# Kernel tuning notes

Measured on AMD Instinct MI355X. Metric: run time of the kernel, lower is better.

Reference implementation:

```python
import jax, jax.numpy as jnp
import numpy as np

FEATURES = 1024
NUM_HEADS = 16
HEAD_DIM = FEATURES // NUM_HEADS


def _cinit(key, shape):
    # complex_xavier_init from the source: std = sqrt(1/(fan_in + fan_out))
    fan_in = int(np.prod(shape[:-1]))
    fan_out = shape[-1]
    std = np.sqrt(1.0 / (fan_in + fan_out)).astype(np.float32)
    return jax.random.normal(key, shape, dtype=jnp.float32) * std


def setup_inputs() -> dict:
    key = jax.random.key(0)
    ks = jax.random.split(key, 12)
    B, S, F = 2, 2048, FEATURES
    inp = {
        'x_r': jax.random.normal(ks[0], (B, S, F), dtype=jnp.float32),
        'x_i': jax.random.normal(ks[1], (B, S, F), dtype=jnp.float32),
        'mask': jnp.ones((B, S), dtype=jnp.float32),
    }
    names = ['q', 'k', 'v', 'o']
    for idx, n in enumerate(names):
        inp[f'W{n}_r'] = _cinit(ks[2 + 2 * idx], (F, F))
        inp[f'W{n}_i'] = _cinit(ks[3 + 2 * idx], (F, F))
        inp[f'b{n}_r'] = jnp.zeros((F,), dtype=jnp.float32)
        inp[f'b{n}_i'] = jnp.zeros((F,), dtype=jnp.float32)
    return inp


def _complex_linear(xr, xi, Wr, Wi, br, bi):
    # (xr + i xi) @ (Wr + i Wi) + (br + i bi)
    yr = xr @ Wr - xi @ Wi + br
    yi = xr @ Wi + xi @ Wr + bi
    return yr, yi


def reference(x_r, x_i, mask,
              Wq_r, Wq_i, bq_r, bq_i,
              Wk_r, Wk_i, bk_r, bk_i,
              Wv_r, Wv_i, bv_r, bv_i,
              Wo_r, Wo_i, bo_r, bo_i):
    B, S, F = x_r.shape
    H, D = NUM_HEADS, HEAD_DIM

    Qr, Qi = _complex_linear(x_r, x_i, Wq_r, Wq_i, bq_r, bq_i)
    Kr, Ki = _complex_linear(x_r, x_i, Wk_r, Wk_i, bk_r, bk_i)
    Vr, Vi = _complex_linear(x_r, x_i, Wv_r, Wv_i, bv_r, bv_i)

    def split_heads(t):  # [B,S,F] -> [B,H,S,D]
        return t.reshape(B, S, H, D).transpose(0, 2, 1, 3)

    Qr, Qi, Kr, Ki, Vr, Vi = map(split_heads, (Qr, Qi, Kr, Ki, Vr, Vi))

    scale = 1.0 / jnp.sqrt(jnp.float32(D))
    # Re(Q K^H) = Qr.Kr + Qi.Ki
    scores = (jnp.einsum('bhqd,bhkd->bhqk', Qr, Kr)
              + jnp.einsum('bhqd,bhkd->bhqk', Qi, Ki)) * scale
    scores = scores + (1.0 - mask[:, None, None, :]) * -1e9
    attn = jax.nn.softmax(scores, axis=-1)  # real-valued weights

    out_r = jnp.einsum('bhqk,bhkd->bhqd', attn, Vr)
    out_i = jnp.einsum('bhqk,bhkd->bhqd', attn, Vi)

    def merge_heads(t):  # [B,H,S,D] -> [B,S,F]
        return t.transpose(0, 2, 1, 3).reshape(B, S, F)

    out_r, out_i = merge_heads(out_r), merge_heads(out_i)
    out_r, out_i = _complex_linear(out_r, out_i, Wo_r, Wo_i, bo_r, bo_i)
    # stack real/imag parts: [2, B, S, F]
    return jnp.stack([out_r, out_i], axis=0)
```

## Files before the change

### kernel.cpp

```cpp
#include <hip/hip_runtime.h>
#include <hip/hip_bf16.h>

typedef unsigned short u16;
typedef unsigned int   u32;
typedef __attribute__((ext_vector_type(8))) short bf16x8;
typedef __attribute__((ext_vector_type(4))) float f32x4;

#define FDIM 1024
#define NH   16
#define HD   64
#define SEQ  2048

#define MFMA16 __builtin_amdgcn_mfma_f32_16x16x32_bf16

__device__ __forceinline__ u16 f2bf(float f) {
    __hip_bfloat16 h = __float2bfloat16(f);
    return *reinterpret_cast<u16*>(&h);
}

__device__ __forceinline__ void g2l16(const u16* g, u16* l) {
    __builtin_amdgcn_global_load_lds(
        (const __attribute__((address_space(1))) unsigned int*)g,
        (__attribute__((address_space(3))) unsigned int*)l,
        16, 0, 0);
}

__global__ __launch_bounds__(256)
void convert_x(const float* __restrict__ xr, const float* __restrict__ xi,
               u16* __restrict__ dr, u16* __restrict__ di)
{
    const long n4 = (long)2 * SEQ * FDIM / 4;
    for (long i = (long)blockIdx.x * blockDim.x + threadIdx.x; i < n4;
         i += (long)gridDim.x * blockDim.x) {
        float4 v = ((const float4*)xr)[i];
        ushort4 o;
        o.x = f2bf(v.x); o.y = f2bf(v.y); o.z = f2bf(v.z); o.w = f2bf(v.w);
        ((ushort4*)dr)[i] = o;
        v = ((const float4*)xi)[i];
        o.x = f2bf(v.x); o.y = f2bf(v.y); o.z = f2bf(v.z); o.w = f2bf(v.w);
        ((ushort4*)di)[i] = o;
    }
}

__global__ __launch_bounds__(256)
void convert_w(const float* __restrict__ W0, const float* __restrict__ W1,
               const float* __restrict__ W2, const float* __restrict__ W3,
               const float* __restrict__ W4, const float* __restrict__ W5,
               const float* __restrict__ W6, const float* __restrict__ W7,
               u16* __restrict__ wt_base)
{
    __shared__ u16 T[64][68];
    const int z = blockIdx.z;
    const float* W = (z == 0) ? W0 : (z == 1) ? W1 : (z == 2) ? W2 : (z == 3) ? W3
                   : (z == 4) ? W4 : (z == 5) ? W5 : (z == 6) ? W6 : W7;
    u16* Wt = wt_base + (long)z * FDIM * FDIM;
    const int n0 = blockIdx.x * 64, k0 = blockIdx.y * 64;
    const int tid = threadIdx.x;
    const int cr = tid & 15, rr = tid >> 4;
    #pragma unroll
    for (int p = 0; p < 4; p++) {
        const int k = p * 16 + rr;
        float4 v = *(const float4*)&W[(long)(k0 + k) * FDIM + n0 + cr * 4];
        T[k][cr*4 + 0] = f2bf(v.x); T[k][cr*4 + 1] = f2bf(v.y);
        T[k][cr*4 + 2] = f2bf(v.z); T[k][cr*4 + 3] = f2bf(v.w);
    }
    __syncthreads();
    #pragma unroll
    for (int p = 0; p < 4; p++) {
        const int n = p * 16 + rr;
        ushort4 o;
        o.x = T[cr*4 + 0][n]; o.y = T[cr*4 + 1][n];
        o.z = T[cr*4 + 2][n]; o.w = T[cr*4 + 3][n];
        *(ushort4*)&Wt[(long)(n0 + n) * FDIM + k0 + cr*4] = o;
    }
}

__global__ __launch_bounds__(256)
void proj_bf16(const u16* __restrict__ Xr_g, const u16* __restrict__ Xi_g,
               const u16* __restrict__ Wt_base,
               const float* __restrict__ bqr, const float* __restrict__ bqi,
               const float* __restrict__ bkr, const float* __restrict__ bki,
               const float* __restrict__ bvr, const float* __restrict__ bvi,
               u16* __restrict__ ws)
{
    __shared__ u16 XsR[2][128 * 32], XsI[2][128 * 32];
    __shared__ u16 WsR[2][128 * 32], WsI[2][128 * 32];

    const int z = blockIdx.z, t = z % 3, b = z / 3;
    const u16* xr = Xr_g + (long)b * SEQ * FDIM;
    const u16* xi = Xi_g + (long)b * SEQ * FDIM;
    const long WT = (long)FDIM * FDIM;
    const u16* wr = Wt_base + (long)(2 * t) * WT;
    const u16* wi = wr + WT;
    const float* br = (t == 0) ? bqr : (t == 1) ? bkr : bvr;
    const float* bi = (t == 0) ? bqi : (t == 1) ? bki : bvi;
    const long TS = (long)2 * SEQ * FDIM;
    u16* outR = ws + (long)(t * 2) * TS + (long)b * SEQ * FDIM;
    u16* outI = outR + TS;

    const int tid = threadIdx.x;
    const int n0  = blockIdx.x * 128;
    const int m0  = blockIdx.y * 128;

    const int lane = tid & 63;
    const int wv   = tid >> 6;
    const int mwo  = (wv >> 1) * 64;
    const int nwo  = (wv & 1) * 64;
    const int ml   = lane & 15;
    const int kg   = lane >> 4;

    const int lr = lane >> 2;
    const int xc = (((lane & 3) ^ (lr & 3)) * 8);
    const int rc = ((kg ^ (ml & 3)) * 8);

    f32x4 accr[4][4], acci[4][4];
    #pragma unroll
    for (int i = 0; i < 4; i++)
        #pragma unroll
        for (int j = 0; j < 4; j++) { accr[i][j] = (f32x4)(0.0f); acci[i][j] = (f32x4)(0.0f); }

    #define PSTAGE(bufi, kk)                                                     \
        do {                                                                     \
            _Pragma("unroll")                                                    \
            for (int sub = 0; sub < 2; sub++) {                                  \
                const int rs  = wv * 32 + sub * 16;                              \
                const int row = rs + lr;                                         \
                g2l16(xr + (long)(m0 + row) * FDIM + (kk) + xc, &XsR[bufi][rs * 32]); \
                g2l16(xi + (long)(m0 + row) * FDIM + (kk) + xc, &XsI[bufi][rs * 32]); \
                g2l16(wr + (long)(n0 + row) * FDIM + (kk) + xc, &WsR[bufi][rs * 32]); \
                g2l16(wi + (long)(n0 + row) * FDIM + (kk) + xc, &WsI[bufi][rs * 32]); \
            }                                                                    \
        } while (0)

    int buf = 0;
    PSTAGE(0, 0);
    __syncthreads();

    for (int k0 = 0; k0 < FDIM; k0 += 32) {
        if (k0 + 32 < FDIM) PSTAGE(buf ^ 1, k0 + 32);

        bf16x8 ar[4], ai[4], nai[4], brf[4], bif[4];
        #pragma unroll
        for (int i = 0; i < 4; i++) {
            ar[i] = *(const bf16x8*)&XsR[buf][(mwo + 16*i + ml) * 32 + rc];
            union { bf16x8 v; u32 w[4]; } u;
            u.v = *(const bf16x8*)&XsI[buf][(mwo + 16*i + ml) * 32 + rc];
            ai[i] = u.v;
            u.w[0] ^= 0x80008000u; u.w[1] ^= 0x80008000u;
            u.w[2] ^= 0x80008000u; u.w[3] ^= 0x80008000u;
            nai[i] = u.v;
        }
        #pragma unroll
        for (int j = 0; j < 4; j++) {
            brf[j] = *(const bf16x8*)&WsR[buf][(nwo + 16*j + ml) * 32 + rc];
            bif[j] = *(const bf16x8*)&WsI[buf][(nwo + 16*j + ml) * 32 + rc];
        }
        #pragma unroll
        for (int i = 0; i < 4; i++)
            #pragma unroll
            for (int j = 0; j < 4; j++) {
                accr[i][j] = MFMA16(ar[i],  brf[j], accr[i][j], 0, 0, 0);
                accr[i][j] = MFMA16(nai[i], bif[j], accr[i][j], 0, 0, 0);
                acci[i][j] = MFMA16(ar[i],  bif[j], acci[i][j], 0, 0, 0);
                acci[i][j] = MFMA16(ai[i],  brf[j], acci[i][j], 0, 0, 0);
            }

        __syncthreads();
        buf ^= 1;
    }
    #undef PSTAGE

    #pragma unroll
    for (int j = 0; j < 4; j++) {
        const int n = n0 + nwo + 16*j + ml;
        const int hh = n >> 6, d = n & 63;
        const float bre = br[n];
        const float bim = bi[n];
        #pragma unroll
        for (int i = 0; i < 4; i++) {
            const int mb = m0 + mwo + 16*i + kg*4;
            if (t < 2) {
                #pragma unroll
                for (int r = 0; r < 4; r++) {
                    const long addr = ((long)hh * SEQ + (mb + r)) * HD + d;
                    outR[addr] = f2bf(accr[i][j][r] + bre);
                    outI[addr] = f2bf(acci[i][j][r] + bim);
                }
            } else {
                const long addr = ((long)hh * HD + d) * SEQ + mb;
                ushort4 vr, vi;
                vr.x = f2bf(accr[i][j][0] + bre); vr.y = f2bf(accr[i][j][1] + bre);
                vr.z = f2bf(accr[i][j][2] + bre); vr.w = f2bf(accr[i][j][3] + bre);
                vi.x = f2bf(acci[i][j][0] + bim); vi.y = f2bf(acci[i][j][1] + bim);
                vi.z = f2bf(acci[i][j][2] + bim); vi.w = f2bf(acci[i][j][3] + bim);
                *(ushort4*)&outR[addr] = vr;
                *(ushort4*)&outI[addr] = vi;
            }
        }
    }
}

__global__ __launch_bounds__(256)
void attn_mfma(const u16* __restrict__ Qr_g, const u16* __restrict__ Qi_g,
               const u16* __restrict__ Kr_g, const u16* __restrict__ Ki_g,
               const u16* __restrict__ Vtr_g, const u16* __restrict__ Vti_g,
               const float* __restrict__ mask_g,
               u16* __restrict__ Ar_g, u16* __restrict__ Ai_g)
{
    __shared__ u16 KT[2][64 * 128];
    __shared__ u16 VT[2][128 * 64];

    const int tid  = threadIdx.x;
    const int lane = tid & 63;
    const int wv   = tid >> 6;
    const int ml   = lane & 15;
    const int quad = lane >> 4;

    const int L   = blockIdx.x + (blockIdx.y << 4) + (blockIdx.z << 8);
    const int xcd = L & 7, qq = L >> 3;
    const int q0  = (qq & 15) * 128;
    const int g   = ((qq >> 4) << 3) | xcd;
    const int h   = g & 15;
    const int b   = g >> 4;
    const long hb  = ((long)b * NH + h) * SEQ * HD;
    const float* mask = mask_g + (long)b * SEQ;

    bf16x8 qf[2][4];
    #pragma unroll
    for (int nt = 0; nt < 2; nt++) {
        const long row = hb + (long)(q0 + wv*32 + nt*16 + ml) * HD;
        qf[nt][0] = *(const bf16x8*)(Qr_g + row + quad*8);
        qf[nt][1] = *(const bf16x8*)(Qr_g + row + 32 + quad*8);
        qf[nt][2] = *(const bf16x8*)(Qi_g + row + quad*8);
        qf[nt][3] = *(const bf16x8*)(Qi_g + row + 32 + quad*8);
    }

    const u16* srcK[4];
    #pragma unroll
    for (int ii = 0; ii < 4; ii++) {
        const int rk = wv*16 + ii*4 + (lane >> 4);
        const int c  = (lane & 15) ^ (rk & 7);
        srcK[ii] = ((c < 8) ? Kr_g : Ki_g) + hb + (long)rk * HD + (c & 7) * 8;
    }
    const u16* srcV[4];
    #pragma unroll
    for (int jj = 0; jj < 4; jj++) {
        const int dv = wv*32 + jj*8 + (lane >> 3);
        const int c  = (lane & 7) ^ (dv & 7);
        srcV[jj] = ((dv < 64) ? Vtr_g : Vti_g) + hb + (long)(dv & 63) * SEQ + c * 8;
    }

    #define STAGE(bufi)                                                         \
        do {                                                                    \
            _Pragma("unroll")                                                   \
            for (int ii = 0; ii < 4; ii++)                                      \
                g2l16(srcK[ii], &KT[bufi][(wv*16 + ii*4) * 128]);               \
            _Pragma("unroll")                                                   \
            for (int jj = 0; jj < 4; jj++)                                      \
                g2l16(srcV[jj], &VT[bufi][(wv*32 + jj*8) * 64]);                \
            _Pragma("unroll")                                                   \
            for (int ii = 0; ii < 4; ii++) srcK[ii] += 64 * HD;                 \
            _Pragma("unroll")                                                   \
            for (int jj = 0; jj < 4; jj++) srcV[jj] += 64;                      \
        } while (0)

    f32x4 oacc[2][8];
    #pragma unroll
    for (int mt = 0; mt < 2; mt++)
        #pragma unroll
        for (int nt = 0; nt < 8; nt++) oacc[mt][nt] = (f32x4)(0.0f);
    float m_run[2] = {-3.0e38f, -3.0e38f};
    float l_run[2] = {0.0f, 0.0f};
    const float scale = 0.125f;

    STAGE(0);
    __syncthreads();

    const int NT = SEQ / 64;
    for (int t = 0; t < NT; ++t) {
        const int cur = t & 1;
        if (t + 1 < NT) STAGE(cur ^ 1);

        f32x4 mrow[4];
        #pragma unroll
        for (int mt = 0; mt < 4; mt++)
            mrow[mt] = *(const f32x4*)(mask + t*64 + mt*16 + quad*4);

        f32x4 sacc[4][2];
        #pragma unroll
        for (int mt = 0; mt < 4; mt++) { sacc[mt][0] = (f32x4)(0.0f); sacc[mt][1] = (f32x4)(0.0f); }
        const u16* Kc = &KT[cur][0];
        __builtin_amdgcn_s_setprio(1);
        #pragma unroll
        for (int mt = 0; mt < 4; mt++)
            #pragma unroll
            for (int kc = 0; kc < 4; kc++) {
                const bf16x8 kf = *(const bf16x8*)
                    &Kc[(mt*16 + ml) * 128 + (((kc*4 + quad) ^ (ml & 7)) * 8)];
                sacc[mt][0] = MFMA16(kf, qf[0][kc], sacc[mt][0], 0, 0, 0);
                sacc[mt][1] = MFMA16(kf, qf[1][kc], sacc[mt][1], 0, 0, 0);
            }
        __builtin_amdgcn_s_setprio(0);

        asm volatile("s_barrier" ::: "memory");

        float md[4][4];
        #pragma unroll
        for (int mt = 0; mt < 4; mt++)
            #pragma unroll
            for (int r = 0; r < 4; r++)
                md[mt][r] = (1.0f - mrow[mt][r]) * -1.0e9f;

        u16* Pb = (u16*)&KT[cur][0];
        float alSave[2];
        #pragma unroll
        for (int nt = 0; nt < 2; nt++) {
            float sv[4][4];
            #pragma unroll
            for (int mt = 0; mt < 4; mt++)
                #pragma unroll
                for (int r = 0; r < 4; r++)
                    sv[mt][r] = sacc[mt][nt][r] * scale + md[mt][r];

            float mA = fmaxf(fmaxf(sv[0][0], sv[0][1]), fmaxf(sv[0][2], sv[0][3]));
            float mB = fmaxf(fmaxf(sv[1][0], sv[1][1]), fmaxf(sv[1][2], sv[1][3]));
            float mC = fmaxf(fmaxf(sv[2][0], sv[2][1]), fmaxf(sv[2][2], sv[2][3]));
            float mD = fmaxf(fmaxf(sv[3][0], sv[3][1]), fmaxf(sv[3][2], sv[3][3]));
            float mx = fmaxf(fmaxf(mA, mB), fmaxf(mC, mD));
            mx = fmaxf(mx, __shfl_xor(mx, 16));
            mx = fmaxf(mx, __shfl_xor(mx, 32));
            const float mn = fmaxf(m_run[nt], mx);
            const float al = __expf(m_run[nt] - mn);

            float p[4][4];
            #pragma unroll
            for (int mt = 0; mt < 4; mt++) {
                p[mt][0] = __expf(sv[mt][0] - mn);
                p[mt][1] = __expf(sv[mt][1] - mn);
                p[mt][2] = __expf(sv[mt][2] - mn);
                p[mt][3] = __expf(sv[mt][3] - mn);
            }
            const int qrow = wv*32 + nt*16 + ml;
            #pragma unroll
            for (int mt = 0; mt < 4; mt++) {
                ushort4 pb;
                pb.x = f2bf(p[mt][0]); pb.y = f2bf(p[mt][1]);
                pb.z = f2bf(p[mt][2]); pb.w = f2bf(p[mt][3]);
                *(ushort4*)&Pb[(long)qrow * 64
                               + (((mt*2 + (quad >> 1)) ^ (ml & 7)) * 8)
                               + (quad & 1) * 4] = pb;
            }
            float s0 = (p[0][0] + p[0][1]) + (p[0][2] + p[0][3]);
            float s1 = (p[1][0] + p[1][1]) + (p[1][2] + p[1][3]);
            float s2 = (p[2][0] + p[2][1]) + (p[2][2] + p[2][3]);
            float s3 = (p[3][0] + p[3][1]) + (p[3][2] + p[3][3]);
            float ps = (s0 + s1) + (s2 + s3);
            ps += __shfl_xor(ps, 16);
            ps += __shfl_xor(ps, 32);
            l_run[nt] = l_run[nt] * al + ps;
            m_run[nt] = mn;
            alSave[nt] = al;
        }

        f32x4 al4[2];
        #pragma unroll
        for (int mt = 0; mt < 2; mt++)
            #pragma unroll
            for (int r = 0; r < 4; r++)
                al4[mt][r] = __shfl(alSave[mt], quad*20 + r);
        #pragma unroll
        for (int mt = 0; mt < 2; mt++)
            #pragma unroll
            for (int nt = 0; nt < 8; nt++) oacc[mt][nt] *= al4[mt];

        const u16* Vc = &VT[cur][0];
        __builtin_amdgcn_s_setprio(1);
        #pragma unroll
        for (int kc = 0; kc < 2; kc++) {
            const int pchunk = ((kc*4 + quad) ^ (ml & 7)) * 8;
            const bf16x8 pf0 = *(const bf16x8*)&Pb[(wv*32 + ml) * 64 + pchunk];
            const bf16x8 pf1 = *(const bf16x8*)&Pb[(wv*32 + 16 + ml) * 64 + pchunk];
            #pragma unroll
            for (int nt = 0; nt < 8; nt++) {
                const bf16x8 vf = *(const bf16x8*)
                    &Vc[(nt*16 + ml) * 64 + (((kc*4 + quad) ^ (ml & 7)) * 8)];
                oacc[0][nt] = MFMA16(pf0, vf, oacc[0][nt], 0, 0, 0);
                oacc[1][nt] = MFMA16(pf1, vf, oacc[1][nt], 0, 0, 0);
            }
        }
        __builtin_amdgcn_s_setprio(0);

        __syncthreads();
    }
    #undef STAGE

    const float linv0 = 1.0f / l_run[0];
    const float linv1 = 1.0f / l_run[1];
    f32x4 li[2];
    #pragma unroll
    for (int r = 0; r < 4; r++) {
        li[0][r] = __shfl(linv0, quad*20 + r);
        li[1][r] = __shfl(linv1, quad*20 + r);
    }
    const long abase = (long)b * SEQ * FDIM;
    #pragma unroll
    for (int mt = 0; mt < 2; mt++)
        #pragma unroll
        for (int nt = 0; nt < 8; nt++) {
            const int dim = nt*16 + ml;
            u16* dst = ((dim < 64) ? Ar_g : Ai_g) + abase
                     + (long)(q0 + wv*32 + mt*16 + quad*4) * FDIM + h * HD + (dim & 63);
            #pragma unroll
            for (int r = 0; r < 4; r++)
                dst[(long)r * FDIM] = f2bf(oacc[mt][nt][r] * li[mt][r]);
        }
}

__global__ __launch_bounds__(256)
void oproj_bf16(const u16* __restrict__ Ar_all, const u16* __restrict__ Ai_all,
                const u16* __restrict__ Wtor,
                const float* __restrict__ bor, const float* __restrict__ boi,
                float* __restrict__ out)
{
    __shared__ u16 XsR[2][128 * 32], XsI[2][128 * 32];
    __shared__ u16 WsR[2][128 * 32], WsI[2][128 * 32];

    const int b = blockIdx.z;
    const u16* ar = Ar_all + (long)b * SEQ * FDIM;
    const u16* ai = Ai_all + (long)b * SEQ * FDIM;
    const u16* wr = Wtor;
    const u16* wi = Wtor + (long)FDIM * FDIM;
    float* outR = out + (long)b * SEQ * FDIM;
    float* outI = out + (long)2 * SEQ * FDIM + (long)b * SEQ * FDIM;

    const int tid = threadIdx.x;
    const int n0  = blockIdx.x * 128;
    const int m0  = blockIdx.y * 128;

    const int lane = tid & 63;
    const int wv   = tid >> 6;
    const int mwo  = (wv >> 1) * 64;
    const int nwo  = (wv & 1) * 64;
    const int ml   = lane & 15;
    const int kg   = lane >> 4;

    const int lr = lane >> 2;
    const int xc = (((lane & 3) ^ (lr & 3)) * 8);
    const int rc = ((kg ^ (ml & 3)) * 8);

    f32x4 accr[4][4], acci[4][4];
    #pragma unroll
    for (int i = 0; i < 4; i++)
        #pragma unroll
        for (int j = 0; j < 4; j++) { accr[i][j] = (f32x4)(0.0f); acci[i][j] = (f32x4)(0.0f); }

    #define OSTAGE(bufi, kk)                                                     \
        do {                                                                     \
            _Pragma("unroll")                                                    \
            for (int sub = 0; sub < 2; sub++) {                                  \
                const int rs  = wv * 32 + sub * 16;                              \
                const int row = rs + lr;                                         \
                g2l16(ar + (long)(m0 + row) * FDIM + (kk) + xc, &XsR[bufi][rs * 32]); \
                g2l16(ai + (long)(m0 + row) * FDIM + (kk) + xc, &XsI[bufi][rs * 32]); \
                g2l16(wr + (long)(n0 + row) * FDIM + (kk) + xc, &WsR[bufi][rs * 32]); \
                g2l16(wi + (long)(n0 + row) * FDIM + (kk) + xc, &WsI[bufi][rs * 32]); \
            }                                                                    \
        } while (0)

    int buf = 0;
    OSTAGE(0, 0);
    __syncthreads();

    for (int k0 = 0; k0 < FDIM; k0 += 32) {
        if (k0 + 32 < FDIM) OSTAGE(buf ^ 1, k0 + 32);

        bf16x8 arf[4], aif[4], naif[4], brf[4], bif[4];
        #pragma unroll
        for (int i = 0; i < 4; i++) {
            arf[i] = *(const bf16x8*)&XsR[buf][(mwo + 16*i + ml) * 32 + rc];
            union { bf16x8 v; u32 w[4]; } u;
            u.v = *(const bf16x8*)&XsI[buf][(mwo + 16*i + ml) * 32 + rc];
            aif[i] = u.v;
            u.w[0] ^= 0x80008000u; u.w[1] ^= 0x80008000u;
            u.w[2] ^= 0x80008000u; u.w[3] ^= 0x80008000u;
            naif[i] = u.v;
        }
        #pragma unroll
        for (int j = 0; j < 4; j++) {
            brf[j] = *(const bf16x8*)&WsR[buf][(nwo + 16*j + ml) * 32 + rc];
            bif[j] = *(const bf16x8*)&WsI[buf][(nwo + 16*j + ml) * 32 + rc];
        }
        #pragma unroll
        for (int i = 0; i < 4; i++)
            #pragma unroll
            for (int j = 0; j < 4; j++) {
                accr[i][j] = MFMA16(arf[i],  brf[j], accr[i][j], 0, 0, 0);
                accr[i][j] = MFMA16(naif[i], bif[j], accr[i][j], 0, 0, 0);
                acci[i][j] = MFMA16(arf[i],  bif[j], acci[i][j], 0, 0, 0);
                acci[i][j] = MFMA16(aif[i],  brf[j], acci[i][j], 0, 0, 0);
            }

        __syncthreads();
        buf ^= 1;
    }
    #undef OSTAGE

    #pragma unroll
    for (int j = 0; j < 4; j++) {
        const int n = n0 + nwo + 16*j + ml;
        const float bre = bor[n];
        const float bim = boi[n];
        #pragma unroll
        for (int i = 0; i < 4; i++) {
            #pragma unroll
            for (int r = 0; r < 4; r++) {
                const int m = m0 + mwo + 16*i + kg*4 + r;
                const long addr = (long)m * FDIM + n;
                outR[addr] = accr[i][j][r] + bre;
                outI[addr] = acci[i][j][r] + bim;
            }
        }
    }
}

extern "C" void kernel_launch(void* const* d_in, const int* in_sizes, int n_in,
                              void* d_out, int out_size, void* d_ws, size_t ws_size,
                              hipStream_t stream)
{
    const float* x_r  = (const float*)d_in[0];
    const float* x_i  = (const float*)d_in[1];
    const float* mask = (const float*)d_in[2];
    const float *Wq_r = (const float*)d_in[3],  *Wq_i = (const float*)d_in[4];
    const float *bq_r = (const float*)d_in[5],  *bq_i = (const float*)d_in[6];
    const float *Wk_r = (const float*)d_in[7],  *Wk_i = (const float*)d_in[8];
    const float *bk_r = (const float*)d_in[9],  *bk_i = (const float*)d_in[10];
    const float *Wv_r = (const float*)d_in[11], *Wv_i = (const float*)d_in[12];
    const float *bv_r = (const float*)d_in[13], *bv_i = (const float*)d_in[14];
    const float *Wo_r = (const float*)d_in[15], *Wo_i = (const float*)d_in[16];
    const float *bo_r = (const float*)d_in[17], *bo_i = (const float*)d_in[18];

    u16* ws = (u16*)d_ws;
    const long TS = (long)2 * SEQ * FDIM;
    const long WT = (long)FDIM * FDIM;
    u16 *Qr = ws,          *Qi = ws + TS;
    u16 *Kr = ws + 2*TS,   *Ki = ws + 3*TS;
    u16 *Vtr = ws + 4*TS,  *Vti = ws + 5*TS;
    u16 *Ar = ws + 6*TS,   *Ai = ws + 7*TS;
    u16 *Xbr = Ar,         *Xbi = Ai;
    u16 *Wt  = ws + 8*TS;

    convert_x<<<dim3(2048), 256, 0, stream>>>(x_r, x_i, Xbr, Xbi);
    convert_w<<<dim3(16, 16, 8), 256, 0, stream>>>(Wq_r, Wq_i, Wk_r, Wk_i,
                                                   Wv_r, Wv_i, Wo_r, Wo_i, Wt);

    proj_bf16<<<dim3(8, 16, 6), 256, 0, stream>>>(Xbr, Xbi, Wt,
        bq_r, bq_i, bk_r, bk_i, bv_r, bv_i, ws);

    attn_mfma<<<dim3(SEQ / 128, NH, 2), 256, 0, stream>>>(Qr, Qi, Kr, Ki, Vtr, Vti,
                                                          mask, Ar, Ai);

    oproj_bf16<<<dim3(8, 16, 2), 256, 0, stream>>>(Ar, Ai, Wt + 6*WT,
                                                   bo_r, bo_i, (float*)d_out);
}
```

Baseline: 490.3 us.

## Use exp2 softmax, LDS mask bias, and skip rescaling when max unchanged

The attention kernel now folds log2(e) into the score scale and uses raw v_exp_f32, precomputing the mask bias once into shared memory instead of loading the mask from global memory every tile. It packs bf16 probabilities with integer rounding and skips the output accumulator rescale when no row's running max grew (wave-uniform check). This targets VALU cost in the softmax section. It adds 8 KB of LDS per block, which could affect occupancy, and adds a branch.

```diff
diff --git a/kernel.cpp b/kernel.cpp
--- a/kernel.cpp
+++ b/kernel.cpp
@@ -23,6 +23,18 @@
         (const __attribute__((address_space(1))) unsigned int*)g,
         (__attribute__((address_space(3))) unsigned int*)l,
         16, 0, 0);
+}
+
+__device__ __forceinline__ float exp2v(float x) {
+    float d;
+    asm("v_exp_f32 %0, %1" : "=v"(d) : "v"(x));
+    return d;
+}
+
+__device__ __forceinline__ u32 bfpack(float a, float b) {
+    u32 ua = __float_as_uint(a), ub = __float_as_uint(b);
+    return ((ua + 0x7FFF + ((ua >> 16) & 1)) >> 16)
+         | ((ub + 0x7FFF + ((ub >> 16) & 1)) & 0xFFFF0000u);
 }
 
 __global__ __launch_bounds__(256)
@@ -209,6 +221,7 @@
 {
     __shared__ u16 KT[2][64 * 128];
     __shared__ u16 VT[2][128 * 64];
+    __shared__ float madd_l[SEQ];
 
     const int tid  = threadIdx.x;
     const int lane = tid & 63;
@@ -271,9 +284,12 @@
         for (int nt = 0; nt < 8; nt++) oacc[mt][nt] = (f32x4)(0.0f);
     float m_run[2] = {-3.0e38f, -3.0e38f};
     float l_run[2] = {0.0f, 0.0f};
-    const float scale = 0.125f;
+    const float SCALE2 = 0.125f * 1.44269504088896f;
 
     STAGE(0);
+    #pragma unroll
+    for (int i = 0; i < SEQ / 256; i++)
+        madd_l[tid + 256 * i] = (1.0f - mask[tid + 256 * i]) * (-1.0e9f * 1.44269504f);
     __syncthreads();
 
     const int NT = SEQ / 64;
@@ -281,10 +297,10 @@
         const int cur = t & 1;
         if (t + 1 < NT) STAGE(cur ^ 1);
 
-        f32x4 mrow[4];
+        f32x4 mdv[4];
         #pragma unroll
         for (int mt = 0; mt < 4; mt++)
-            mrow[mt] = *(const f32x4*)(mask + t*64 + mt*16 + quad*4);
+            mdv[mt] = *(const f32x4*)&madd_l[t*64 + mt*16 + quad*4];
 
         f32x4 sacc[4][2];
         #pragma unroll
@@ -304,15 +320,9 @@
 
         asm volatile("s_barrier" ::: "memory");
 
-        float md[4][4];
-        #pragma unroll
-        for (int mt = 0; mt < 4; mt++)
-            #pragma unroll
-            for (int r = 0; r < 4; r++)
-                md[mt][r] = (1.0f - mrow[mt][r]) * -1.0e9f;
-
         u16* Pb = (u16*)&KT[cur][0];
         float alSave[2];
+        int need = 0;
         #pragma unroll
         for (int nt = 0; nt < 2; nt++) {
             float sv[4][4];
@@ -320,7 +330,7 @@
             for (int mt = 0; mt < 4; mt++)
                 #pragma unroll
                 for (int r = 0; r < 4; r++)
-                    sv[mt][r] = sacc[mt][nt][r] * scale + md[mt][r];
+                    sv[mt][r] = sacc[mt][nt][r] * SCALE2 + mdv[mt][r];
 
             float mA = fmaxf(fmaxf(sv[0][0], sv[0][1]), fmaxf(sv[0][2], sv[0][3]));
             float mB = fmaxf(fmaxf(sv[1][0], sv[1][1]), fmaxf(sv[1][2], sv[1][3]));
@@ -329,26 +339,30 @@
             float mx = fmaxf(fmaxf(mA, mB), fmaxf(mC, mD));
             mx = fmaxf(mx, __shfl_xor(mx, 16));
             mx = fmaxf(mx, __shfl_xor(mx, 32));
-            const float mn = fmaxf(m_run[nt], mx);
-            const float al = __expf(m_run[nt] - mn);
+
+            const int grow = __any(mx > m_run[nt]);
+            float mn, al;
+            if (grow) { mn = fmaxf(m_run[nt], mx); al = exp2v(m_run[nt] - mn); }
+            else      { mn = m_run[nt];            al = 1.0f; }
+            need |= grow;
 
             float p[4][4];
             #pragma unroll
             for (int mt = 0; mt < 4; mt++) {
-                p[mt][0] = __expf(sv[mt][0] - mn);
-                p[mt][1] = __expf(sv[mt][1] - mn);
-                p[mt][2] = __expf(sv[mt][2] - mn);
-                p[mt][3] = __expf(sv[mt][3] - mn);
+                p[mt][0] = exp2v(sv[mt][0] - mn);
+                p[mt][1] = exp2v(sv[mt][1] - mn);
+                p[mt][2] = exp2v(sv[mt][2] - mn);
+                p[mt][3] = exp2v(sv[mt][3] - mn);
             }
             const int qrow = wv*32 + nt*16 + ml;
             #pragma unroll
             for (int mt = 0; mt < 4; mt++) {
-                ushort4 pb;
-                pb.x = f2bf(p[mt][0]); pb.y = f2bf(p[mt][1]);
-                pb.z = f2bf(p[mt][2]); pb.w = f2bf(p[mt][3]);
-                *(ushort4*)&Pb[(long)qrow * 64
-                               + (((mt*2 + (quad >> 1)) ^ (ml & 7)) * 8)
-                               + (quad & 1) * 4] = pb;
+                uint2 pw;
+                pw.x = bfpack(p[mt][0], p[mt][1]);
+                pw.y = bfpack(p[mt][2], p[mt][3]);
+                *(uint2*)&Pb[(long)qrow * 64
+                             + (((mt*2 + (quad >> 1)) ^ (ml & 7)) * 8)
+                             + (quad & 1) * 4] = pw;
             }
             float s0 = (p[0][0] + p[0][1]) + (p[0][2] + p[0][3]);
             float s1 = (p[1][0] + p[1][1]) + (p[1][2] + p[1][3]);
@@ -362,16 +376,18 @@
             alSave[nt] = al;
         }
 
-        f32x4 al4[2];
-        #pragma unroll
-        for (int mt = 0; mt < 2; mt++)
-            #pragma unroll
-            for (int r = 0; r < 4; r++)
-                al4[mt][r] = __shfl(alSave[mt], quad*20 + r);
-        #pragma unroll
-        for (int mt = 0; mt < 2; mt++)
-            #pragma unroll
-            for (int nt = 0; nt < 8; nt++) oacc[mt][nt] *= al4[mt];
+        if (need) {
+            f32x4 al4[2];
+            #pragma unroll
+            for (int mt = 0; mt < 2; mt++)
+                #pragma unroll
+                for (int r = 0; r < 4; r++)
+                    al4[mt][r] = __shfl(alSave[mt], quad*20 + r);
+            #pragma unroll
+            for (int mt = 0; mt < 2; mt++)
+                #pragma unroll
+                for (int nt = 0; nt < 8; nt++) oacc[mt][nt] *= al4[mt];
+        }
 
         const u16* Vc = &VT[cur][0];
         __builtin_amdgcn_s_setprio(1);
```

After: 503.3 us. +2.6%, slower.

## Halve attention query tile and drop LDS double buffering to raise occupancy

Applied to the files above, without the earlier changes.

The attention kernel now gives each wave 16 query rows instead of 32, so each block covers 64 queries and the grid doubles. The K/V staging buffers go from double to single, halving LDS per block, and launch bounds request 4 blocks per CU. The goal is more resident waves to hide memory and MFMA latency in place of explicit prefetch. In exchange the next K/V tile is no longer loaded during compute, an extra barrier is added per iteration, and K/V tiles are reloaded twice as often in total.

```diff
diff --git a/kernel.cpp b/kernel.cpp
--- a/kernel.cpp
+++ b/kernel.cpp
@@ -200,15 +200,15 @@
     }
 }
 
-__global__ __launch_bounds__(256)
+__global__ __launch_bounds__(256, 4)
 void attn_mfma(const u16* __restrict__ Qr_g, const u16* __restrict__ Qi_g,
                const u16* __restrict__ Kr_g, const u16* __restrict__ Ki_g,
                const u16* __restrict__ Vtr_g, const u16* __restrict__ Vti_g,
                const float* __restrict__ mask_g,
                u16* __restrict__ Ar_g, u16* __restrict__ Ai_g)
 {
-    __shared__ u16 KT[2][64 * 128];
-    __shared__ u16 VT[2][128 * 64];
+    __shared__ u16 KT[64 * 128];
+    __shared__ u16 VT[128 * 64];
 
     const int tid  = threadIdx.x;
     const int lane = tid & 63;
@@ -216,23 +216,22 @@
     const int ml   = lane & 15;
     const int quad = lane >> 4;
 
-    const int L   = blockIdx.x + (blockIdx.y << 4) + (blockIdx.z << 8);
+    const int L   = blockIdx.x + (blockIdx.y << 5) + (blockIdx.z << 9);
     const int xcd = L & 7, qq = L >> 3;
-    const int q0  = (qq & 15) * 128;
-    const int g   = ((qq >> 4) << 3) | xcd;
+    const int q0  = (qq & 31) * 64;
+    const int g   = ((qq >> 5) << 3) | xcd;
     const int h   = g & 15;
     const int b   = g >> 4;
     const long hb  = ((long)b * NH + h) * SEQ * HD;
     const float* mask = mask_g + (long)b * SEQ;
 
-    bf16x8 qf[2][4];
-    #pragma unroll
-    for (int nt = 0; nt < 2; nt++) {
-        const long row = hb + (long)(q0 + wv*32 + nt*16 + ml) * HD;
-        qf[nt][0] = *(const bf16x8*)(Qr_g + row + quad*8);
-        qf[nt][1] = *(const bf16x8*)(Qr_g + row + 32 + quad*8);
-        qf[nt][2] = *(const bf16x8*)(Qi_g + row + quad*8);
-        qf[nt][3] = *(const bf16x8*)(Qi_g + row + 32 + quad*8);
+    bf16x8 qf[4];
+    {
+        const long row = hb + (long)(q0 + wv*16 + ml) * HD;
+        qf[0] = *(const bf16x8*)(Qr_g + row + quad*8);
+        qf[1] = *(const bf16x8*)(Qr_g + row + 32 + quad*8);
+        qf[2] = *(const bf16x8*)(Qi_g + row + quad*8);
+        qf[3] = *(const bf16x8*)(Qi_g + row + 32 + quad*8);
     }
 
     const u16* srcK[4];
@@ -250,170 +249,139 @@
         srcV[jj] = ((dv < 64) ? Vtr_g : Vti_g) + hb + (long)(dv & 63) * SEQ + c * 8;
     }
 
-    #define STAGE(bufi)                                                         \
+    #define STAGE()                                                             \
         do {                                                                    \
             _Pragma("unroll")                                                   \
             for (int ii = 0; ii < 4; ii++)                                      \
-                g2l16(srcK[ii], &KT[bufi][(wv*16 + ii*4) * 128]);               \
+                g2l16(srcK[ii], &KT[(wv*16 + ii*4) * 128]);                     \
             _Pragma("unroll")                                                   \
             for (int jj = 0; jj < 4; jj++)                                      \
-                g2l16(srcV[jj], &VT[bufi][(wv*32 + jj*8) * 64]);                \
+                g2l16(srcV[jj], &VT[(wv*32 + jj*8) * 64]);                      \
             _Pragma("unroll")                                                   \
             for (int ii = 0; ii < 4; ii++) srcK[ii] += 64 * HD;                 \
             _Pragma("unroll")                                                   \
             for (int jj = 0; jj < 4; jj++) srcV[jj] += 64;                      \
         } while (0)
 
-    f32x4 oacc[2][8];
-    #pragma unroll
-    for (int mt = 0; mt < 2; mt++)
-        #pragma unroll
-        for (int nt = 0; nt < 8; nt++) oacc[mt][nt] = (f32x4)(0.0f);
-    float m_run[2] = {-3.0e38f, -3.0e38f};
-    float l_run[2] = {0.0f, 0.0f};
+    f32x4 oacc[8];
+    #pragma unroll
+    for (int nt = 0; nt < 8; nt++) oacc[nt] = (f32x4)(0.0f);
+    float m_run = -3.0e38f;
+    float l_run = 0.0f;
     const float scale = 0.125f;
-
-    STAGE(0);
-    __syncthreads();
 
     const int NT = SEQ / 64;
     for (int t = 0; t < NT; ++t) {
-        const int cur = t & 1;
-        if (t + 1 < NT) STAGE(cur ^ 1);
+        if (t) __syncthreads();
+        STAGE();
 
         f32x4 mrow[4];
         #pragma unroll
         for (int mt = 0; mt < 4; mt++)
             mrow[mt] = *(const f32x4*)(mask + t*64 + mt*16 + quad*4);
 
-        f32x4 sacc[4][2];
-        #pragma unroll
-        for (int mt = 0; mt < 4; mt++) { sacc[mt][0] = (f32x4)(0.0f); sacc[mt][1] = (f32x4)(0.0f); }
-        const u16* Kc = &KT[cur][0];
+        __syncthreads();
+
+        f32x4 sacc[4];
+        #pragma unroll
+        for (int mt = 0; mt < 4; mt++) sacc[mt] = (f32x4)(0.0f);
         __builtin_amdgcn_s_setprio(1);
         #pragma unroll
         for (int mt = 0; mt < 4; mt++)
             #pragma unroll
             for (int kc = 0; kc < 4; kc++) {
                 const bf16x8 kf = *(const bf16x8*)
-                    &Kc[(mt*16 + ml) * 128 + (((kc*4 + quad) ^ (ml & 7)) * 8)];
-                sacc[mt][0] = MFMA16(kf, qf[0][kc], sacc[mt][0], 0, 0, 0);
-                sacc[mt][1] = MFMA16(kf, qf[1][kc], sacc[mt][1], 0, 0, 0);
+                    &KT[(mt*16 + ml) * 128 + (((kc*4 + quad) ^ (ml & 7)) * 8)];
+                sacc[mt] = MFMA16(kf, qf[kc], sacc[mt], 0, 0, 0);
             }
         __builtin_amdgcn_s_setprio(0);
 
         asm volatile("s_barrier" ::: "memory");
 
-        float md[4][4];
+        u16* Pb = (u16*)&KT[0];
+        float sv[4][4];
         #pragma unroll
         for (int mt = 0; mt < 4; mt++)
             #pragma unroll
             for (int r = 0; r < 4; r++)
-                md[mt][r] = (1.0f - mrow[mt][r]) * -1.0e9f;
-
-        u16* Pb = (u16*)&KT[cur][0];
-        float alSave[2];
-        #pragma unroll
-        for (int nt = 0; nt < 2; nt++) {
-            float sv[4][4];
-            #pragma unroll
-            for (int mt = 0; mt < 4; mt++)
-                #pragma unroll
-                for (int r = 0; r < 4; r++)
-                    sv[mt][r] = sacc[mt][nt][r] * scale + md[mt][r];
-
-            float mA = fmaxf(fmaxf(sv[0][0], sv[0][1]), fmaxf(sv[0][2], sv[0][3]));
-            float mB = fmaxf(fmaxf(sv[1][0], sv[1][1]), fmaxf(sv[1][2], sv[1][3]));
-            float mC = fmaxf(fmaxf(sv[2][0], sv[2][1]), fmaxf(sv[2][2], sv[2][3]));
-            float mD = fmaxf(fmaxf(sv[3][0], sv[3][1]), fmaxf(sv[3][2], sv[3][3]));
-            float mx = fmaxf(fmaxf(mA, mB), fmaxf(mC, mD));
-            mx = fmaxf(mx, __shfl_xor(mx, 16));
-            mx = fmaxf(mx, __shfl_xor(mx, 32));
-            const float mn = fmaxf(m_run[nt], mx);
-            const float al = __expf(m_run[nt] - mn);
-
-            float p[4][4];
-            #pragma unroll
-            for (int mt = 0; mt < 4; mt++) {
-                p[mt][0] = __expf(sv[mt][0] - mn);
-                p[mt][1] = __expf(sv[mt][1] - mn);
-                p[mt][2] = __expf(sv[mt][2] - mn);
-                p[mt][3] = __expf(sv[mt][3] - mn);
-            }
-            const int qrow = wv*32 + nt*16 + ml;
-            #pragma unroll
-            for (int mt = 0; mt < 4; mt++) {
-                ushort4 pb;
-                pb.x = f2bf(p[mt][0]); pb.y = f2bf(p[mt][1]);
-                pb.z = f2bf(p[mt][2]); pb.w = f2bf(p[mt][3]);
-                *(ushort4*)&Pb[(long)qrow * 64
-                               + (((mt*2 + (quad >> 1)) ^ (ml & 7)) * 8)
-                               + (quad & 1) * 4] = pb;
-            }
-            float s0 = (p[0][0] + p[0][1]) + (p[0][2] + p[0][3]);
-            float s1 = (p[1][0] + p[1][1]) + (p[1][2] + p[1][3]);
-            float s2 = (p[2][0] + p[2][1]) + (p[2][2] + p[2][3]);
-            float s3 = (p[3][0] + p[3][1]) + (p[3][2] + p[3][3]);
-            float ps = (s0 + s1) + (s2 + s3);
-            ps += __shfl_xor(ps, 16);
-            ps += __shfl_xor(ps, 32);
-            l_run[nt] = l_run[nt] * al + ps;
-            m_run[nt] = mn;
-            alSave[nt] = al;
-        }
-
-        f32x4 al4[2];
-        #pragma unroll
-        for (int mt = 0; mt < 2; mt++)
-            #pragma unroll
-            for (int r = 0; r < 4; r++)
-                al4[mt][r] = __shfl(alSave[mt], quad*20 + r);
-        #pragma unroll
-        for (int mt = 0; mt < 2; mt++)
-            #pragma unroll
-            for (int nt = 0; nt < 8; nt++) oacc[mt][nt] *= al4[mt];
-
-        const u16* Vc = &VT[cur][0];
+                sv[mt][r] = sacc[mt][r] * scale + (1.0f - mrow[mt][r]) * -1.0e9f;
+
+        float mA = fmaxf(fmaxf(sv[0][0], sv[0][1]), fmaxf(sv[0][2], sv[0][3]));
+        float mB = fmaxf(fmaxf(sv[1][0], sv[1][1]), fmaxf(sv[1][2], sv[1][3]));
+        float mC = fmaxf(fmaxf(sv[2][0], sv[2][1]), fmaxf(sv[2][2], sv[2][3]));
+        float mD = fmaxf(fmaxf(sv[3][0], sv[3][1]), fmaxf(sv[3][2], sv[3][3]));
+        float mx = fmaxf(fmaxf(mA, mB), fmaxf(mC, mD));
+        mx = fmaxf(mx, __shfl_xor(mx, 16));
+        mx = fmaxf(mx, __shfl_xor(mx, 32));
+        const float mn = fmaxf(m_run, mx);
+        const float al = __expf(m_run - mn);
+
+        float p[4][4];
+        #pragma unroll
+        for (int mt = 0; mt < 4; mt++) {
+            p[mt][0] = __expf(sv[mt][0] - mn);
+            p[mt][1] = __expf(sv[mt][1] - mn);
+            p[mt][2] = __expf(sv[mt][2] - mn);
+            p[mt][3] = __expf(sv[mt][3] - mn);
+        }
+        const int qrow = wv*16 + ml;
+        #pragma unroll
+        for (int mt = 0; mt < 4; mt++) {
+            ushort4 pb;
+            pb.x = f2bf(p[mt][0]); pb.y = f2bf(p[mt][1]);
+            pb.z = f2bf(p[mt][2]); pb.w = f2bf(p[mt][3]);
+            *(ushort4*)&Pb[(long)qrow * 64
+                           + (((mt*2 + (quad >> 1)) ^ (ml & 7)) * 8)
+                           + (quad & 1) * 4] = pb;
+        }
+        float s0 = (p[0][0] + p[0][1]) + (p[0][2] + p[0][3]);
+        float s1 = (p[1][0] + p[1][1]) + (p[1][2] + p[1][3]);
+        float s2 = (p[2][0] + p[2][1]) + (p[2][2] + p[2][3]);
+        float s3 = (p[3][0] + p[3][1]) + (p[3][2] + p[3][3]);
+        float ps = (s0 + s1) + (s2 + s3);
+        ps += __shfl_xor(ps, 16);
+        ps += __shfl_xor(ps, 32);
+        l_run = l_run * al + ps;
+        m_run = mn;
+
+        f32x4 al4;
+        #pragma unroll
+        for (int r = 0; r < 4; r++)
+            al4[r] = __shfl(al, quad*20 + r);
+        #pragma unroll
+        for (int nt = 0; nt < 8; nt++) oacc[nt] *= al4;
+
         __builtin_amdgcn_s_setprio(1);
         #pragma unroll
         for (int kc = 0; kc < 2; kc++) {
             const int pchunk = ((kc*4 + quad) ^ (ml & 7)) * 8;
-            const bf16x8 pf0 = *(const bf16x8*)&Pb[(wv*32 + ml) * 64 + pchunk];
-            const bf16x8 pf1 = *(const bf16x8*)&Pb[(wv*32 + 16 + ml) * 64 + pchunk];
+            const bf16x8 pf = *(const bf16x8*)&Pb[(long)qrow * 64 + pchunk];
             #pragma unroll
             for (int nt = 0; nt < 8; nt++) {
                 const bf16x8 vf = *(const bf16x8*)
-                    &Vc[(nt*16 + ml) * 64 + (((kc*4 + quad) ^ (ml & 7)) * 8)];
-                oacc[0][nt] = MFMA16(pf0, vf, oacc[0][nt], 0, 0, 0);
-                oacc[1][nt] = MFMA16(pf1, vf, oacc[1][nt], 0, 0, 0);
+                    &VT[(nt*16 + ml) * 64 + (((kc*4 + quad) ^ (ml & 7)) * 8)];
+                oacc[nt] = MFMA16(pf, vf, oacc[nt], 0, 0, 0);
             }
         }
         __builtin_amdgcn_s_setprio(0);
-
-        __syncthreads();
     }
     #undef STAGE
 
-    const float linv0 = 1.0f / l_run[0];
-    const float linv1 = 1.0f / l_run[1];
-    f32x4 li[2];
-    #pragma unroll
-    for (int r = 0; r < 4; r++) {
-        li[0][r] = __shfl(linv0, quad*20 + r);
-        li[1][r] = __shfl(linv1, quad*20 + r);
-    }
+    const float linv = 1.0f / l_run;
+    f32x4 li;
+    #pragma unroll
+    for (int r = 0; r < 4; r++)
+        li[r] = __shfl(linv, quad*20 + r);
     const long abase = (long)b * SEQ * FDIM;
     #pragma unroll
-    for (int mt = 0; mt < 2; mt++)
-        #pragma unroll
-        for (int nt = 0; nt < 8; nt++) {
-            const int dim = nt*16 + ml;
-            u16* dst = ((dim < 64) ? Ar_g : Ai_g) + abase
-                     + (long)(q0 + wv*32 + mt*16 + quad*4) * FDIM + h * HD + (dim & 63);
-            #pragma unroll
-            for (int r = 0; r < 4; r++)
-                dst[(long)r * FDIM] = f2bf(oacc[mt][nt][r] * li[mt][r]);
-        }
+    for (int nt = 0; nt < 8; nt++) {
+        const int dim = nt*16 + ml;
+        u16* dst = ((dim < 64) ? Ar_g : Ai_g) + abase
+                 + (long)(q0 + wv*16 + quad*4) * FDIM + h * HD + (dim & 63);
+        #pragma unroll
+        for (int r = 0; r < 4; r++)
+            dst[(long)r * FDIM] = f2bf(oacc[nt][r] * li[r]);
+    }
 }
 
 __global__ __launch_bounds__(256)
@@ -556,8 +524,8 @@
     proj_bf16<<<dim3(8, 16, 6), 256, 0, stream>>>(Xbr, Xbi, Wt,
         bq_r, bq_i, bk_r, bk_i, bv_r, bv_i, ws);
 
-    attn_mfma<<<dim3(SEQ / 128, NH, 2), 256, 0, stream>>>(Qr, Qi, Kr, Ki, Vtr, Vti,
-                                                          mask, Ar, Ai);
+    attn_mfma<<<dim3(SEQ / 64, NH, 2), 256, 0, stream>>>(Qr, Qi, Kr, Ki, Vtr, Vti,
+                                                         mask, Ar, Ai);
 
     oproj_bf16<<<dim3(8, 16, 2), 256, 0, stream>>>(Ar, Ai, Wt + 6*WT,
                                                    bo_r, bo_i, (float*)d_out);
```

Measured after the change: 450.2 us. 1.09x faster.
